# Kernel optimization log

Hardware: AMD Instinct MI355X
Metric: run time of the kernel (lower is better)

Reference implementation:

```python
import jax, jax.numpy as jnp
import numpy as np

B, IN_CH, OUT_CH, K, H, W = 1, 64, 64, 4, 512, 512
N = H * W  # per-pixel sampling: one point per output pixel


def setup_inputs() -> dict:
    key = jax.random.key(0)
    ks = jax.random.split(key, 9)
    inp = {
        "input": jax.random.normal(ks[0], (B, IN_CH, H, W), dtype=jnp.float32),
        "ax": jax.random.uniform(ks[1], (B, N), dtype=jnp.float32) * (W - 1),
        "ay": jax.random.uniform(ks[2], (B, N), dtype=jnp.float32) * (H - 1),
        # 1x1 conv params (kernel is [out,in] since kh=kw=1)
        "conv_w": jax.random.normal(ks[3], (OUT_CH, IN_CH), dtype=jnp.float32) * 0.05,
        "conv_b": jax.random.normal(ks[4], (OUT_CH,), dtype=jnp.float32) * 0.05,
        "offset_w": jax.random.normal(ks[5], (K, 2, IN_CH), dtype=jnp.float32) * 0.05,
        "offset_b": jax.random.normal(ks[6], (K, 2), dtype=jnp.float32) * 0.05,
        "wconv_w": jax.random.normal(ks[7], (K, IN_CH), dtype=jnp.float32) * 0.05,
        "wconv_b": jax.random.normal(ks[8], (K,), dtype=jnp.float32) * 0.05,
    }
    return inp


def _bilinear(feat, xs, ys):
    """feat [C,H,W]; xs, ys [m] pixel coords; bilinear, zero padding. -> [C,m]."""
    C, Hh, Ww = feat.shape
    x0f = jnp.floor(xs)
    y0f = jnp.floor(ys)
    wx = xs - x0f
    wy = ys - y0f
    x0 = x0f.astype(jnp.int32)
    y0 = y0f.astype(jnp.int32)
    out = jnp.zeros((C, xs.shape[0]), dtype=feat.dtype)
    corners = ((0, 0, (1 - wx) * (1 - wy)), (1, 0, wx * (1 - wy)),
               (0, 1, (1 - wx) * wy), (1, 1, wx * wy))
    for dx, dy, wgt in corners:
        xc = x0 + dx
        yc = y0 + dy
        valid = (xc >= 0) & (xc < Ww) & (yc >= 0) & (yc < Hh)
        v = feat[:, jnp.clip(yc, 0, Hh - 1), jnp.clip(xc, 0, Ww - 1)]  # [C,m]
        out = out + v * (wgt * valid)[None, :]
    return out


def reference(input, ax, ay, conv_w, conv_b, offset_w, offset_b, wconv_w, wconv_b):
    b, c, h, w = input.shape
    k = offset_w.shape[0]
    n = ax.shape[1]  # == h*w
    # 1x1 convs as einsums
    proj = jnp.einsum('bchw,oc->bohw', input, conv_w) + conv_b[None, :, None, None]
    flows = jnp.einsum('bchw,kdc->bkdhw', input, offset_w) + offset_b[None, :, :, None, None]  # [b,k,2,h,w]
    weights = jax.nn.softmax(
        jnp.einsum('bchw,kc->bkhw', input, wconv_w) + wconv_b[None, :, None, None], axis=1)  # [b,k,h,w]
    # gather flow at truncated integer coords (flow[num, iy, ix, :])
    ix = jnp.trunc(ax).astype(jnp.int32)  # [b,n]
    iy = jnp.trunc(ay).astype(jnp.int32)
    flow_pts = jax.vmap(lambda fl, i, j: fl[:, :, j, i])(flows, ix, iy)  # [b,k,2,n]
    vx = ax[:, None, :] + flow_pts[:, :, 0]  # [b,k,n]
    vy = ay[:, None, :] + flow_pts[:, :, 1]
    # torch normalizes align_corners=True-style then grid_sample (align_corners=False) unnormalizes:
    # pixel = v * W/(W-1) - 0.5
    xs = vx * (w / (w - 1)) - 0.5
    ys = vy * (h / (h - 1)) - 0.5
    samp = jax.vmap(lambda f, x, y: _bilinear(f, x.reshape(-1), y.reshape(-1)))(proj, xs, ys)  # [b,C,k*n]
    feats = samp.reshape(b, proj.shape[1], k, h, w).transpose(0, 2, 1, 3, 4)  # [b,k,C,h,w]
    return (weights[:, :, None, :, :] * feats).sum(axis=1)  # [b,out_ch,h,w]
```

## Files before the change

kernel.cpp:

```cpp
#include <hip/hip_runtime.h>
#include <hip/hip_bf16.h>

#define NPIX (512 * 512)
#define IMW 512
#define IMH 512

typedef float fvec4 __attribute__((ext_vector_type(4)));

static __device__ __forceinline__ unsigned short f2bf(float f) {
  union { __hip_bfloat16 h; unsigned short u; } cv;
  cv.h = __float2bfloat16(f);
  return cv.u;
}

static __device__ __forceinline__ unsigned pack2bf(float lo, float hi) {
  return (unsigned)f2bf(lo) | ((unsigned)f2bf(hi) << 16);
}

__global__ __launch_bounds__(256) void k1_pointwise(
    const float* __restrict__ in, const float* __restrict__ conv_w,
    const float* __restrict__ conv_b, const float* __restrict__ offset_w,
    const float* __restrict__ offset_b, const float* __restrict__ wconv_w,
    const float* __restrict__ wconv_b, __hip_bfloat16* __restrict__ proj_t,
    float* __restrict__ flows_t, float* __restrict__ wts_t) {
  const int n = blockIdx.x * 256 + threadIdx.x;

#pragma unroll 1
  for (int half = 0; half < 2; ++half) {
    const float* wbase = conv_w + half * 32 * 64;
    const float* bbase = conv_b + half * 32;
    float acc[32];
#pragma unroll
    for (int o = 0; o < 32; ++o) acc[o] = bbase[o];
#pragma unroll 1
    for (int cb = 0; cb < 64; cb += 8) {
      float x[8];
#pragma unroll
      for (int j = 0; j < 8; ++j) x[j] = in[(size_t)(cb + j) * NPIX + n];
#pragma unroll
      for (int o = 0; o < 32; ++o) {
#pragma unroll
        for (int j = 0; j < 8; ++j)
          acc[o] = fmaf(x[j], wbase[o * 64 + cb + j], acc[o]);
      }
    }
    uint4* pj = (uint4*)(proj_t + (size_t)n * 64 + half * 32);
    uint4 v0, v1, v2, v3;
    v0.x = pack2bf(acc[0], acc[1]);   v0.y = pack2bf(acc[2], acc[3]);
    v0.z = pack2bf(acc[4], acc[5]);   v0.w = pack2bf(acc[6], acc[7]);
    v1.x = pack2bf(acc[8], acc[9]);   v1.y = pack2bf(acc[10], acc[11]);
    v1.z = pack2bf(acc[12], acc[13]); v1.w = pack2bf(acc[14], acc[15]);
    v2.x = pack2bf(acc[16], acc[17]); v2.y = pack2bf(acc[18], acc[19]);
    v2.z = pack2bf(acc[20], acc[21]); v2.w = pack2bf(acc[22], acc[23]);
    v3.x = pack2bf(acc[24], acc[25]); v3.y = pack2bf(acc[26], acc[27]);
    v3.z = pack2bf(acc[28], acc[29]); v3.w = pack2bf(acc[30], acc[31]);
    pj[0] = v0; pj[1] = v1; pj[2] = v2; pj[3] = v3;
  }

  {
    float acc[12];
#pragma unroll
    for (int o = 0; o < 8; ++o) acc[o] = offset_b[o];
#pragma unroll
    for (int o = 0; o < 4; ++o) acc[8 + o] = wconv_b[o];
#pragma unroll 1
    for (int cb = 0; cb < 64; cb += 8) {
      float x[8];
#pragma unroll
      for (int j = 0; j < 8; ++j) x[j] = in[(size_t)(cb + j) * NPIX + n];
#pragma unroll
      for (int o = 0; o < 8; ++o) {
#pragma unroll
        for (int j = 0; j < 8; ++j)
          acc[o] = fmaf(x[j], offset_w[o * 64 + cb + j], acc[o]);
      }
#pragma unroll
      for (int o = 0; o < 4; ++o) {
#pragma unroll
        for (int j = 0; j < 8; ++j)
          acc[8 + o] = fmaf(x[j], wconv_w[o * 64 + cb + j], acc[8 + o]);
      }
    }
    float4* fl4 = (float4*)(flows_t + (size_t)n * 8);
    fl4[0] = make_float4(acc[0], acc[1], acc[2], acc[3]);
    fl4[1] = make_float4(acc[4], acc[5], acc[6], acc[7]);

    const float m = fmaxf(fmaxf(acc[8], acc[9]), fmaxf(acc[10], acc[11]));
    const float e0 = __expf(acc[8] - m), e1 = __expf(acc[9] - m);
    const float e2 = __expf(acc[10] - m), e3 = __expf(acc[11] - m);
    const float inv = 1.f / (e0 + e1 + e2 + e3);
    *(float4*)(wts_t + (size_t)n * 4) =
        make_float4(e0 * inv, e1 * inv, e2 * inv, e3 * inv);
  }
}

static __device__ __forceinline__ void sample_one(
    float axv, float ayv, float4 f01, float4 f23, float4 wk4,
    const __hip_bfloat16* __restrict__ proj_t, int l8,
    float* __restrict__ dst) {
  const float fx[4] = {f01.x, f01.z, f23.x, f23.z};
  const float fy[4] = {f01.y, f01.w, f23.y, f23.w};
  const float wk[4] = {wk4.x, wk4.y, wk4.z, wk4.w};

  float acc[8];
#pragma unroll
  for (int j = 0; j < 8; ++j) acc[j] = 0.f;

#pragma unroll
  for (int k = 0; k < 4; ++k) {
    const float xs = (axv + fx[k]) * (512.f / 511.f) - 0.5f;
    const float ys = (ayv + fy[k]) * (512.f / 511.f) - 0.5f;
    const float x0f = floorf(xs), y0f = floorf(ys);
    const float wx = xs - x0f, wy = ys - y0f;
    const int x0 = (int)x0f, y0 = (int)y0f;
    const int x1 = x0 + 1, y1 = y0 + 1;
    const int cx0 = min(max(x0, 0), IMW - 1);
    const int cx1 = min(max(x1, 0), IMW - 1);
    const int cy0 = min(max(y0, 0), IMH - 1);
    const int cy1 = min(max(y1, 0), IMH - 1);
    const float vx0 = (x0 >= 0 && x0 < IMW) ? 1.f : 0.f;
    const float vx1 = (x1 >= 0 && x1 < IMW) ? 1.f : 0.f;
    const float vy0 = (y0 >= 0 && y0 < IMH) ? 1.f : 0.f;
    const float vy1 = (y1 >= 0 && y1 < IMH) ? 1.f : 0.f;
    const float s00 = wk[k] * (1.f - wx) * (1.f - wy) * vx0 * vy0;
    const float s10 = wk[k] * wx * (1.f - wy) * vx1 * vy0;
    const float s01 = wk[k] * (1.f - wx) * wy * vx0 * vy1;
    const float s11 = wk[k] * wx * wy * vx1 * vy1;

    const uint4 u00 = *(const uint4*)(proj_t + (size_t)(cy0 * IMW + cx0) * 64 + l8 * 8);
    const uint4 u10 = *(const uint4*)(proj_t + (size_t)(cy0 * IMW + cx1) * 64 + l8 * 8);
    const uint4 u01 = *(const uint4*)(proj_t + (size_t)(cy1 * IMW + cx0) * 64 + l8 * 8);
    const uint4 u11 = *(const uint4*)(proj_t + (size_t)(cy1 * IMW + cx1) * 64 + l8 * 8);

    const unsigned w00[4] = {u00.x, u00.y, u00.z, u00.w};
    const unsigned w10[4] = {u10.x, u10.y, u10.z, u10.w};
    const unsigned w01[4] = {u01.x, u01.y, u01.z, u01.w};
    const unsigned w11[4] = {u11.x, u11.y, u11.z, u11.w};
#pragma unroll
    for (int q = 0; q < 4; ++q) {
      acc[2 * q] = fmaf(__uint_as_float(w00[q] << 16), s00, acc[2 * q]);
      acc[2 * q] = fmaf(__uint_as_float(w10[q] << 16), s10, acc[2 * q]);
      acc[2 * q] = fmaf(__uint_as_float(w01[q] << 16), s01, acc[2 * q]);
      acc[2 * q] = fmaf(__uint_as_float(w11[q] << 16), s11, acc[2 * q]);
      acc[2 * q + 1] = fmaf(__uint_as_float(w00[q] & 0xffff0000u), s00, acc[2 * q + 1]);
      acc[2 * q + 1] = fmaf(__uint_as_float(w10[q] & 0xffff0000u), s10, acc[2 * q + 1]);
      acc[2 * q + 1] = fmaf(__uint_as_float(w01[q] & 0xffff0000u), s01, acc[2 * q + 1]);
      acc[2 * q + 1] = fmaf(__uint_as_float(w11[q] & 0xffff0000u), s11, acc[2 * q + 1]);
    }
  }
  *(float4*)(dst) = make_float4(acc[0], acc[1], acc[2], acc[3]);
  *(float4*)(dst + 4) = make_float4(acc[4], acc[5], acc[6], acc[7]);
}

__global__ __launch_bounds__(256) void k2_sample(
    const float* __restrict__ ax, const float* __restrict__ ay,
    const __hip_bfloat16* __restrict__ proj_t,
    const float* __restrict__ flows_t, const float* __restrict__ wts_t,
    float* __restrict__ out) {
  __shared__ float tile[64][68];
  const int t = threadIdx.x;
  const int g8 = t >> 3;
  const int l8 = t & 7;
  const int p0 = blockIdx.x * 64;
  const int pA = p0 + g8;
  const int pB = p0 + 32 + g8;

  const float axA = ax[pA], ayA = ay[pA];
  const float axB = ax[pB], ayB = ay[pB];
  const float4 wkA = *(const float4*)(wts_t + (size_t)pA * 4);
  const float4 wkB = *(const float4*)(wts_t + (size_t)pB * 4);
  const size_t nA = (size_t)((int)ayA * IMW + (int)axA);
  const size_t nB = (size_t)((int)ayB * IMW + (int)axB);
  const float4 fA01 = *(const float4*)(flows_t + nA * 8);
  const float4 fA23 = *(const float4*)(flows_t + nA * 8 + 4);
  const float4 fB01 = *(const float4*)(flows_t + nB * 8);
  const float4 fB23 = *(const float4*)(flows_t + nB * 8 + 4);

  sample_one(axA, ayA, fA01, fA23, wkA, proj_t, l8, &tile[g8][8 * l8]);
  sample_one(axB, ayB, fB01, fB23, wkB, proj_t, l8, &tile[32 + g8][8 * l8]);
  __syncthreads();

  const int g16 = t >> 4;
  const int l16 = t & 15;
#pragma unroll
  for (int it = 0; it < 4; ++it) {
    const int c = it * 16 + g16;
    fvec4 vv;
    vv.x = tile[4 * l16 + 0][c];
    vv.y = tile[4 * l16 + 1][c];
    vv.z = tile[4 * l16 + 2][c];
    vv.w = tile[4 * l16 + 3][c];
    __builtin_nontemporal_store(
        vv, (fvec4*)(out + (size_t)c * NPIX + p0 + 4 * l16));
  }
}

extern "C" void kernel_launch(void* const* d_in, const int* in_sizes, int n_in,
                              void* d_out, int out_size, void* d_ws,
                              size_t ws_size, hipStream_t stream) {
  const float* input = (const float*)d_in[0];
  const float* ax = (const float*)d_in[1];
  const float* ay = (const float*)d_in[2];
  const float* conv_w = (const float*)d_in[3];
  const float* conv_b = (const float*)d_in[4];
  const float* offset_w = (const float*)d_in[5];
  const float* offset_b = (const float*)d_in[6];
  const float* wconv_w = (const float*)d_in[7];
  const float* wconv_b = (const float*)d_in[8];
  float* out = (float*)d_out;

  __hip_bfloat16* proj_t = (__hip_bfloat16*)d_ws;
  float* flows_t = (float*)(proj_t + (size_t)NPIX * 64);
  float* wts_t = flows_t + (size_t)NPIX * 8;

  hipLaunchKernelGGL(k1_pointwise, dim3(NPIX / 256), dim3(256), 0, stream,
                     input, conv_w, conv_b, offset_w, offset_b, wconv_w,
                     wconv_b, proj_t, flows_t, wts_t);
  hipLaunchKernelGGL(k2_sample, dim3(NPIX / 64), dim3(256), 0, stream, ax, ay,
                     proj_t, flows_t, wts_t, out);
}
```

Baseline: 247.6 us.

## Compute 1x1 projection with bf16 MFMA and store flows in bf16

```diff
diff --git a/kernel.cpp b/kernel.cpp
--- a/kernel.cpp
+++ b/kernel.cpp
@@ -6,100 +6,134 @@
 #define IMH 512
 
 typedef float fvec4 __attribute__((ext_vector_type(4)));
+typedef short bf16x8 __attribute__((ext_vector_type(8)));
+typedef float f32x4 __attribute__((ext_vector_type(4)));
 
 static __device__ __forceinline__ unsigned short f2bf(float f) {
   union { __hip_bfloat16 h; unsigned short u; } cv;
   cv.h = __float2bfloat16(f);
   return cv.u;
 }
-
 static __device__ __forceinline__ unsigned pack2bf(float lo, float hi) {
   return (unsigned)f2bf(lo) | ((unsigned)f2bf(hi) << 16);
 }
-
-__global__ __launch_bounds__(256) void k1_pointwise(
+static __device__ __forceinline__ float bflo(unsigned u) {
+  return __uint_as_float(u << 16);
+}
+static __device__ __forceinline__ float bfhi(unsigned u) {
+  return __uint_as_float(u & 0xffff0000u);
+}
+
+__global__ __launch_bounds__(256) void k1_proj_mfma(
     const float* __restrict__ in, const float* __restrict__ conv_w,
-    const float* __restrict__ conv_b, const float* __restrict__ offset_w,
+    const float* __restrict__ conv_b, __hip_bfloat16* __restrict__ proj_t) {
+  const int wave = threadIdx.x >> 6;
+  const int l = threadIdx.x & 63;
+  const int px0 = blockIdx.x * 64 + wave * 16;
+  const int lc = l & 15;
+  const int kg = l >> 4;
+
+  bf16x8 bf[2][4];
+#pragma unroll
+  for (int t = 0; t < 2; ++t) {
+#pragma unroll
+    for (int nt = 0; nt < 4; ++nt) {
+      const float* wr = conv_w + (size_t)(nt * 16 + lc) * 64 + t * 32 + kg * 8;
+      const float4 w0 = *(const float4*)(wr);
+      const float4 w1 = *(const float4*)(wr + 4);
+      bf16x8 f;
+      f[0] = (short)f2bf(w0.x); f[1] = (short)f2bf(w0.y);
+      f[2] = (short)f2bf(w0.z); f[3] = (short)f2bf(w0.w);
+      f[4] = (short)f2bf(w1.x); f[5] = (short)f2bf(w1.y);
+      f[6] = (short)f2bf(w1.z); f[7] = (short)f2bf(w1.w);
+      bf[t][nt] = f;
+    }
+  }
+
+  f32x4 acc[4];
+#pragma unroll
+  for (int nt = 0; nt < 4; ++nt) {
+    const float b = conv_b[nt * 16 + lc];
+    f32x4 c; c[0] = b; c[1] = b; c[2] = b; c[3] = b;
+    acc[nt] = c;
+  }
+
+#pragma unroll
+  for (int t = 0; t < 2; ++t) {
+    bf16x8 af;
+#pragma unroll
+    for (int j = 0; j < 8; ++j) {
+      const float xv = in[(size_t)(t * 32 + kg * 8 + j) * NPIX + px0 + lc];
+      af[j] = (short)f2bf(xv);
+    }
+#pragma unroll
+    for (int nt = 0; nt < 4; ++nt)
+      acc[nt] =
+          __builtin_amdgcn_mfma_f32_16x16x32_bf16(af, bf[t][nt], acc[nt], 0, 0, 0);
+  }
+
+#pragma unroll
+  for (int nt = 0; nt < 4; ++nt) {
+#pragma unroll
+    for (int r = 0; r < 4; ++r) {
+      const int px = px0 + kg * 4 + r;
+      union { __hip_bfloat16 h; unsigned short u; } cv;
+      cv.u = f2bf(acc[nt][r]);
+      proj_t[(size_t)px * 64 + nt * 16 + lc] = cv.h;
+    }
+  }
+}
+
+__global__ __launch_bounds__(256) void k1_flows(
+    const float* __restrict__ in, const float* __restrict__ offset_w,
     const float* __restrict__ offset_b, const float* __restrict__ wconv_w,
-    const float* __restrict__ wconv_b, __hip_bfloat16* __restrict__ proj_t,
-    float* __restrict__ flows_t, float* __restrict__ wts_t) {
+    const float* __restrict__ wconv_b, __hip_bfloat16* __restrict__ flows_t,
+    float* __restrict__ wts_t) {
   const int n = blockIdx.x * 256 + threadIdx.x;
-
+  float acc[12];
+#pragma unroll
+  for (int o = 0; o < 8; ++o) acc[o] = offset_b[o];
+#pragma unroll
+  for (int o = 0; o < 4; ++o) acc[8 + o] = wconv_b[o];
 #pragma unroll 1
-  for (int half = 0; half < 2; ++half) {
-    const float* wbase = conv_w + half * 32 * 64;
-    const float* bbase = conv_b + half * 32;
-    float acc[32];
-#pragma unroll
-    for (int o = 0; o < 32; ++o) acc[o] = bbase[o];
-#pragma unroll 1
-    for (int cb = 0; cb < 64; cb += 8) {
-      float x[8];
-#pragma unroll
-      for (int j = 0; j < 8; ++j) x[j] = in[(size_t)(cb + j) * NPIX + n];
-#pragma unroll
-      for (int o = 0; o < 32; ++o) {
-#pragma unroll
-        for (int j = 0; j < 8; ++j)
-          acc[o] = fmaf(x[j], wbase[o * 64 + cb + j], acc[o]);
-      }
-    }
-    uint4* pj = (uint4*)(proj_t + (size_t)n * 64 + half * 32);
-    uint4 v0, v1, v2, v3;
-    v0.x = pack2bf(acc[0], acc[1]);   v0.y = pack2bf(acc[2], acc[3]);
-    v0.z = pack2bf(acc[4], acc[5]);   v0.w = pack2bf(acc[6], acc[7]);
-    v1.x = pack2bf(acc[8], acc[9]);   v1.y = pack2bf(acc[10], acc[11]);
-    v1.z = pack2bf(acc[12], acc[13]); v1.w = pack2bf(acc[14], acc[15]);
-    v2.x = pack2bf(acc[16], acc[17]); v2.y = pack2bf(acc[18], acc[19]);
-    v2.z = pack2bf(acc[20], acc[21]); v2.w = pack2bf(acc[22], acc[23]);
-    v3.x = pack2bf(acc[24], acc[25]); v3.y = pack2bf(acc[26], acc[27]);
-    v3.z = pack2bf(acc[28], acc[29]); v3.w = pack2bf(acc[30], acc[31]);
-    pj[0] = v0; pj[1] = v1; pj[2] = v2; pj[3] = v3;
-  }
-
-  {
-    float acc[12];
-#pragma unroll
-    for (int o = 0; o < 8; ++o) acc[o] = offset_b[o];
-#pragma unroll
-    for (int o = 0; o < 4; ++o) acc[8 + o] = wconv_b[o];
-#pragma unroll 1
-    for (int cb = 0; cb < 64; cb += 8) {
-      float x[8];
-#pragma unroll
-      for (int j = 0; j < 8; ++j) x[j] = in[(size_t)(cb + j) * NPIX + n];
-#pragma unroll
-      for (int o = 0; o < 8; ++o) {
-#pragma unroll
-        for (int j = 0; j < 8; ++j)
-          acc[o] = fmaf(x[j], offset_w[o * 64 + cb + j], acc[o]);
-      }
-#pragma unroll
-      for (int o = 0; o < 4; ++o) {
-#pragma unroll
-        for (int j = 0; j < 8; ++j)
-          acc[8 + o] = fmaf(x[j], wconv_w[o * 64 + cb + j], acc[8 + o]);
-      }
-    }
-    float4* fl4 = (float4*)(flows_t + (size_t)n * 8);
-    fl4[0] = make_float4(acc[0], acc[1], acc[2], acc[3]);
-    fl4[1] = make_float4(acc[4], acc[5], acc[6], acc[7]);
-
-    const float m = fmaxf(fmaxf(acc[8], acc[9]), fmaxf(acc[10], acc[11]));
-    const float e0 = __expf(acc[8] - m), e1 = __expf(acc[9] - m);
-    const float e2 = __expf(acc[10] - m), e3 = __expf(acc[11] - m);
-    const float inv = 1.f / (e0 + e1 + e2 + e3);
-    *(float4*)(wts_t + (size_t)n * 4) =
-        make_float4(e0 * inv, e1 * inv, e2 * inv, e3 * inv);
-  }
+  for (int cb = 0; cb < 64; cb += 8) {
+    float x[8];
+#pragma unroll
+    for (int j = 0; j < 8; ++j) x[j] = in[(size_t)(cb + j) * NPIX + n];
+#pragma unroll
+    for (int o = 0; o < 8; ++o) {
+#pragma unroll
+      for (int j = 0; j < 8; ++j)
+        acc[o] = fmaf(x[j], offset_w[o * 64 + cb + j], acc[o]);
+    }
+#pragma unroll
+    for (int o = 0; o < 4; ++o) {
+#pragma unroll
+      for (int j = 0; j < 8; ++j)
+        acc[8 + o] = fmaf(x[j], wconv_w[o * 64 + cb + j], acc[8 + o]);
+    }
+  }
+  uint4 fv;
+  fv.x = pack2bf(acc[0], acc[1]);
+  fv.y = pack2bf(acc[2], acc[3]);
+  fv.z = pack2bf(acc[4], acc[5]);
+  fv.w = pack2bf(acc[6], acc[7]);
+  *(uint4*)(flows_t + (size_t)n * 8) = fv;
+
+  const float m = fmaxf(fmaxf(acc[8], acc[9]), fmaxf(acc[10], acc[11]));
+  const float e0 = __expf(acc[8] - m), e1 = __expf(acc[9] - m);
+  const float e2 = __expf(acc[10] - m), e3 = __expf(acc[11] - m);
+  const float inv = 1.f / (e0 + e1 + e2 + e3);
+  *(float4*)(wts_t + (size_t)n * 4) =
+      make_float4(e0 * inv, e1 * inv, e2 * inv, e3 * inv);
 }
 
 static __device__ __forceinline__ void sample_one(
-    float axv, float ayv, float4 f01, float4 f23, float4 wk4,
+    float axv, float ayv, uint4 fw, float4 wk4,
     const __hip_bfloat16* __restrict__ proj_t, int l8,
     float* __restrict__ dst) {
-  const float fx[4] = {f01.x, f01.z, f23.x, f23.z};
-  const float fy[4] = {f01.y, f01.w, f23.y, f23.w};
+  const float fx[4] = {bflo(fw.x), bflo(fw.y), bflo(fw.z), bflo(fw.w)};
+  const float fy[4] = {bfhi(fw.x), bfhi(fw.y), bfhi(fw.z), bfhi(fw.w)};
   const float wk[4] = {wk4.x, wk4.y, wk4.z, wk4.w};
 
   float acc[8];
@@ -138,14 +172,14 @@
     const unsigned w11[4] = {u11.x, u11.y, u11.z, u11.w};
 #pragma unroll
     for (int q = 0; q < 4; ++q) {
-      acc[2 * q] = fmaf(__uint_as_float(w00[q] << 16), s00, acc[2 * q]);
-      acc[2 * q] = fmaf(__uint_as_float(w10[q] << 16), s10, acc[2 * q]);
-      acc[2 * q] = fmaf(__uint_as_float(w01[q] << 16), s01, acc[2 * q]);
-      acc[2 * q] = fmaf(__uint_as_float(w11[q] << 16), s11, acc[2 * q]);
-      acc[2 * q + 1] = fmaf(__uint_as_float(w00[q] & 0xffff0000u), s00, acc[2 * q + 1]);
-      acc[2 * q + 1] = fmaf(__uint_as_float(w10[q] & 0xffff0000u), s10, acc[2 * q + 1]);
-      acc[2 * q + 1] = fmaf(__uint_as_float(w01[q] & 0xffff0000u), s01, acc[2 * q + 1]);
-      acc[2 * q + 1] = fmaf(__uint_as_float(w11[q] & 0xffff0000u), s11, acc[2 * q + 1]);
+      acc[2 * q] = fmaf(bflo(w00[q]), s00, acc[2 * q]);
+      acc[2 * q] = fmaf(bflo(w10[q]), s10, acc[2 * q]);
+      acc[2 * q] = fmaf(bflo(w01[q]), s01, acc[2 * q]);
+      acc[2 * q] = fmaf(bflo(w11[q]), s11, acc[2 * q]);
+      acc[2 * q + 1] = fmaf(bfhi(w00[q]), s00, acc[2 * q + 1]);
+      acc[2 * q + 1] = fmaf(bfhi(w10[q]), s10, acc[2 * q + 1]);
+      acc[2 * q + 1] = fmaf(bfhi(w01[q]), s01, acc[2 * q + 1]);
+      acc[2 * q + 1] = fmaf(bfhi(w11[q]), s11, acc[2 * q + 1]);
     }
   }
   *(float4*)(dst) = make_float4(acc[0], acc[1], acc[2], acc[3]);
@@ -155,8 +189,8 @@
 __global__ __launch_bounds__(256) void k2_sample(
     const float* __restrict__ ax, const float* __restrict__ ay,
     const __hip_bfloat16* __restrict__ proj_t,
-    const float* __restrict__ flows_t, const float* __restrict__ wts_t,
-    float* __restrict__ out) {
+    const __hip_bfloat16* __restrict__ flows_t,
+    const float* __restrict__ wts_t, float* __restrict__ out) {
   __shared__ float tile[64][68];
   const int t = threadIdx.x;
   const int g8 = t >> 3;
@@ -171,13 +205,11 @@
   const float4 wkB = *(const float4*)(wts_t + (size_t)pB * 4);
   const size_t nA = (size_t)((int)ayA * IMW + (int)axA);
   const size_t nB = (size_t)((int)ayB * IMW + (int)axB);
-  const float4 fA01 = *(const float4*)(flows_t + nA * 8);
-  const float4 fA23 = *(const float4*)(flows_t + nA * 8 + 4);
-  const float4 fB01 = *(const float4*)(flows_t + nB * 8);
-  const float4 fB23 = *(const float4*)(flows_t + nB * 8 + 4);
-
-  sample_one(axA, ayA, fA01, fA23, wkA, proj_t, l8, &tile[g8][8 * l8]);
-  sample_one(axB, ayB, fB01, fB23, wkB, proj_t, l8, &tile[32 + g8][8 * l8]);
+  const uint4 fwA = *(const uint4*)(flows_t + nA * 8);
+  const uint4 fwB = *(const uint4*)(flows_t + nB * 8);
+
+  sample_one(axA, ayA, fwA, wkA, proj_t, l8, &tile[g8][8 * l8]);
+  sample_one(axB, ayB, fwB, wkB, proj_t, l8, &tile[32 + g8][8 * l8]);
   __syncthreads();
 
   const int g16 = t >> 4;
@@ -210,12 +242,13 @@
   float* out = (float*)d_out;
 
   __hip_bfloat16* proj_t = (__hip_bfloat16*)d_ws;
-  float* flows_t = (float*)(proj_t + (size_t)NPIX * 64);
-  float* wts_t = flows_t + (size_t)NPIX * 8;
-
-  hipLaunchKernelGGL(k1_pointwise, dim3(NPIX / 256), dim3(256), 0, stream,
-                     input, conv_w, conv_b, offset_w, offset_b, wconv_w,
-                     wconv_b, proj_t, flows_t, wts_t);
+  __hip_bfloat16* flows_t = proj_t + (size_t)NPIX * 64;
+  float* wts_t = (float*)(flows_t + (size_t)NPIX * 8);
+
+  hipLaunchKernelGGL(k1_proj_mfma, dim3(NPIX / 64), dim3(256), 0, stream,
+                     input, conv_w, conv_b, proj_t);
+  hipLaunchKernelGGL(k1_flows, dim3(NPIX / 256), dim3(256), 0, stream, input,
+                     offset_w, offset_b, wconv_w, wconv_b, flows_t, wts_t);
   hipLaunchKernelGGL(k2_sample, dim3(NPIX / 64), dim3(256), 0, stream, ax, ay,
                      proj_t, flows_t, wts_t, out);
 }
```

Result: faster. 213.7 us (-13.7%).
